# Kernel optimization log

Measured on AMD Instinct MI355X. Metric: run time of the kernel, lower is better.

Reference implementation:

```python
import jax, jax.numpy as jnp
import numpy as np

WINDOW = 33  # must match init_kwargs window_size (odd)


def setup_inputs() -> dict:
    key = jax.random.key(0)
    kq, kk, kv, km = jax.random.split(key, 4)
    B, S, D = 4, 2048, 256
    query = jax.random.normal(kq, (B, S, D), dtype=jnp.float32)
    k = jax.random.normal(kk, (B, S, D), dtype=jnp.float32)
    value = jax.random.normal(kv, (B, S, D), dtype=jnp.float32)
    mask = jax.random.randint(km, (B, S), 0, 2).astype(jnp.int32)
    return {"query": query, "key": k, "value": value, "mask": mask}


def reference(query, key, value, mask):
    # Local (sliding-window) attention, window centered at each position.
    B, S, D = query.shape
    half = WINDOW // 2
    offs = jnp.arange(-half, half + 1)                 # [W]
    idx = jnp.arange(S)[:, None] + offs[None, :]       # [S, W]
    valid = (idx >= 0) & (idx < S)                     # in-bounds window entries
    idxc = jnp.clip(idx, 0, S - 1)
    k_win = key[:, idxc]                               # [B, S, W, D]
    v_win = value[:, idxc]                             # [B, S, W, D]
    scores = jnp.einsum('bsd,bswd->bsw', query, k_win) / jnp.sqrt(jnp.float32(D))
    m_win = (mask[:, idxc] != 0) & valid[None]         # [B, S, W]
    scores = jnp.where(m_win, scores, jnp.float32(-1e10))  # masked_fill(-1e10)
    p_attn = jax.nn.softmax(scores, axis=-1)           # [B, S, W]
    values = jnp.einsum('bsw,bswd->bsd', p_attn, v_win)
    return values, p_attn
```

## Files before the change

kernel.cpp:

```cpp
#include <hip/hip_runtime.h>

#define S_LEN 2048
#define D_DIM 256
#define WIN 33
#define HALF 16
#define TROWS 16
#define SPAN 48
#define SC_STRIDE 68
#define PT_STRIDE 72

typedef __attribute__((ext_vector_type(8))) short short8_t;
typedef __attribute__((ext_vector_type(4))) float f32x4;

__device__ inline unsigned short f32_to_bf16(float f) {
    unsigned u = __float_as_uint(f);
    return (unsigned short)((u + 0x7fffu + ((u >> 16) & 1u)) >> 16);
}
__device__ inline unsigned pack2_bf16(float lo, float hi) {
    unsigned a = __float_as_uint(lo) + 0x8000u;
    unsigned b = __float_as_uint(hi) + 0x8000u;
    return __builtin_amdgcn_perm(b, a, 0x07060302);
}
__device__ inline short8_t pack_bf16x8(float4 x, float4 y) {
    union { unsigned u[4]; short8_t s; } r;
    r.u[0] = pack2_bf16(x.x, x.y); r.u[1] = pack2_bf16(x.z, x.w);
    r.u[2] = pack2_bf16(y.x, y.y); r.u[3] = pack2_bf16(y.z, y.w);
    return r.s;
}

__global__ __launch_bounds__(512) void local_attn_v7(
    const float* __restrict__ q,
    const float* __restrict__ k,
    const float* __restrict__ v,
    const int*   __restrict__ mask,
    float* __restrict__ out_v,
    float* __restrict__ out_p)
{
    __shared__ __align__(16) float          Sc[TROWS * SC_STRIDE];
    __shared__ __align__(16) unsigned short Pt[TROWS * PT_STRIDE];
    __shared__ int wm[SPAN];

    const int t    = threadIdx.x;
    const int lane = t & 63;
    const int w    = t >> 6;
    const int l15  = lane & 15;
    const int q4   = lane >> 4;

    const int bid  = blockIdx.x;
    const int tile = ((bid & 7) << 6) | (bid >> 3);
    const int b    = tile >> 7;
    const int s0   = (tile & 127) << 4;

    const float* qb = q + ((size_t)b * S_LEN + s0) * D_DIM;
    const float* kb = k + (size_t)b * S_LEN * D_DIM;
    const float* vb = v + (size_t)b * S_LEN * D_DIM;

    if (t < SPAN) {
        const int idx = s0 - HALF + t;
        wm[t] = (idx >= 0 && idx < S_LEN) ? (mask[b * S_LEN + idx] != 0) : 0;
    }

    if (w < 3) {
        const int c    = 16 * w + l15;
        const int kidx = min(max(s0 - HALF + c, 0), S_LEN - 1);
        const float* kr = kb + (size_t)kidx * D_DIM;
        const float* qr = qb + (size_t)l15 * D_DIM;
        f32x4 acc = (f32x4){0.f, 0.f, 0.f, 0.f};
#pragma unroll
        for (int ks = 0; ks < 8; ++ks) {
            const float* pq = qr + ks * 32 + q4 * 8;
            const float* pk = kr + ks * 32 + q4 * 8;
            const short8_t aq = pack_bf16x8(*(const float4*)pq, *(const float4*)(pq + 4));
            const short8_t bk = pack_bf16x8(*(const float4*)pk, *(const float4*)(pk + 4));
            acc = __builtin_amdgcn_mfma_f32_16x16x32_bf16(aq, bk, acc, 0, 0, 0);
        }
#pragma unroll
        for (int r = 0; r < 4; ++r)
            Sc[(q4 * 4 + r) * SC_STRIDE + c] = acc[r];
    }

    short8_t bv[2][2];
    {
        const bool act1 = (q4 < 2);
        const short8_t zfrag = {0,0,0,0,0,0,0,0};
        float vr[2][2][8];
#pragma unroll
        for (int nt = 0; nt < 2; ++nt) {
            const int d = 32 * w + nt * 16 + l15;
#pragma unroll
            for (int j = 0; j < 8; ++j) {
                const int g0   = q4 * 8 + j;
                const int idx0 = min(max(s0 - HALF + g0, 0), S_LEN - 1);
                vr[nt][0][j] = vb[(size_t)idx0 * D_DIM + d];
            }
            if (act1) {
#pragma unroll
                for (int j = 0; j < 8; ++j) {
                    const int g1   = 32 + q4 * 8 + j;
                    const int idx1 = min(max(s0 - HALF + g1, 0), S_LEN - 1);
                    vr[nt][1][j] = vb[(size_t)idx1 * D_DIM + d];
                }
            }
        }
#pragma unroll
        for (int nt = 0; nt < 2; ++nt) {
            float4 x, y;
            x.x = vr[nt][0][0]; x.y = vr[nt][0][1]; x.z = vr[nt][0][2]; x.w = vr[nt][0][3];
            y.x = vr[nt][0][4]; y.y = vr[nt][0][5]; y.z = vr[nt][0][6]; y.w = vr[nt][0][7];
            bv[nt][0] = pack_bf16x8(x, y);
            if (act1) {
                x.x = vr[nt][1][0]; x.y = vr[nt][1][1]; x.z = vr[nt][1][2]; x.w = vr[nt][1][3];
                y.x = vr[nt][1][4]; y.y = vr[nt][1][5]; y.z = vr[nt][1][6]; y.w = vr[nt][1][7];
                bv[nt][1] = pack_bf16x8(x, y);
            } else {
                bv[nt][1] = zfrag;
            }
        }
    }
    __syncthreads();

    {
        const int row = t >> 5;
        const int e   = t & 31;
        float vs[2];
#pragma unroll
        for (int kq = 0; kq < 2; ++kq) {
            const int c = 2 * e + kq;
            const int j = c - row;
            const bool inb = (j >= 0) && (j < WIN) && (c < SPAN);
            vs[kq] = inb ? (wm[c < SPAN ? c : 0] ? Sc[row * SC_STRIDE + (c < SPAN ? c : 0)] * 0.0625f
                                                 : -1e10f)
                         : -1e30f;
        }
        float m = fmaxf(vs[0], vs[1]);
        m = fmaxf(m, __shfl_xor(m, 1, 64));
        m = fmaxf(m, __shfl_xor(m, 2, 64));
        m = fmaxf(m, __shfl_xor(m, 4, 64));
        m = fmaxf(m, __shfl_xor(m, 8, 64));
        m = fmaxf(m, __shfl_xor(m, 16, 64));
        float s = 0.f;
#pragma unroll
        for (int kq = 0; kq < 2; ++kq) { vs[kq] = __expf(vs[kq] - m); s += vs[kq]; }
        s += __shfl_xor(s, 1, 64);
        s += __shfl_xor(s, 2, 64);
        s += __shfl_xor(s, 4, 64);
        s += __shfl_xor(s, 8, 64);
        s += __shfl_xor(s, 16, 64);
        const float rinv = 1.0f / s;

        float p0 = vs[0] * rinv, p1 = vs[1] * rinv;
        *(unsigned*)&Pt[row * PT_STRIDE + 2 * e] = pack2_bf16(p0, p1);
        float* prow = out_p + ((size_t)(b * S_LEN + s0 + row)) * WIN;
        const int j0 = 2 * e - row;
        if (j0 >= 0 && j0 < WIN)     prow[j0]     = p0;
        if (j0 + 1 >= 0 && j0 + 1 < WIN) prow[j0 + 1] = p1;
    }
    __syncthreads();

    {
        const short8_t ap0 = *(const short8_t*)&Pt[l15 * PT_STRIDE + q4 * 8];
        const short8_t ap1 = *(const short8_t*)&Pt[l15 * PT_STRIDE + 32 + q4 * 8];
        float* ob = out_v + ((size_t)b * S_LEN + s0) * D_DIM;
#pragma unroll
        for (int nt = 0; nt < 2; ++nt) {
            f32x4 acc = (f32x4){0.f, 0.f, 0.f, 0.f};
            acc = __builtin_amdgcn_mfma_f32_16x16x32_bf16(ap0, bv[nt][0], acc, 0, 0, 0);
            acc = __builtin_amdgcn_mfma_f32_16x16x32_bf16(ap1, bv[nt][1], acc, 0, 0, 0);
            const int d = 32 * w + nt * 16 + l15;
#pragma unroll
            for (int r = 0; r < 4; ++r)
                ob[(size_t)(q4 * 4 + r) * D_DIM + d] = acc[r];
        }
    }
}

extern "C" void kernel_launch(void* const* d_in, const int* in_sizes, int n_in,
                              void* d_out, int out_size, void* d_ws, size_t ws_size,
                              hipStream_t stream) {
    const float* q    = (const float*)d_in[0];
    const float* k    = (const float*)d_in[1];
    const float* v    = (const float*)d_in[2];
    const int*   mask = (const int*)d_in[3];

    const int B = 4;
    float* out_v = (float*)d_out;
    float* out_p = (float*)d_out + (size_t)B * S_LEN * D_DIM;

    const int blocks = B * (S_LEN / TROWS);
    local_attn_v7<<<blocks, 512, 0, stream>>>(q, k, v, mask, out_v, out_p);
}
```

Before: 83.31 us.

## Overlap V loads with softmax via LDS-only barriers and interior fast path

Replaces __syncthreads with a barrier that waits only on LDS traffic, so V global loads issued before the softmax stay in flight across it. The bf16 packing of V moves to after the softmax, where the data is first needed. Interior tiles get a separate path without index clamping, and launch bounds now request 4 blocks per CU. This is meant to hide global-load latency behind the score and softmax work, at the cost of more live registers holding raw V values and a duplicated code path.

```diff
diff --git a/kernel.cpp b/kernel.cpp
--- a/kernel.cpp
+++ b/kernel.cpp
@@ -12,10 +12,6 @@
 typedef __attribute__((ext_vector_type(8))) short short8_t;
 typedef __attribute__((ext_vector_type(4))) float f32x4;
 
-__device__ inline unsigned short f32_to_bf16(float f) {
-    unsigned u = __float_as_uint(f);
-    return (unsigned short)((u + 0x7fffu + ((u >> 16) & 1u)) >> 16);
-}
 __device__ inline unsigned pack2_bf16(float lo, float hi) {
     unsigned a = __float_as_uint(lo) + 0x8000u;
     unsigned b = __float_as_uint(hi) + 0x8000u;
@@ -28,7 +24,11 @@
     return r.s;
 }
 
-__global__ __launch_bounds__(512) void local_attn_v7(
+__device__ inline void lds_barrier() {
+    asm volatile("s_waitcnt lgkmcnt(0)\n\ts_barrier" ::: "memory");
+}
+
+__global__ __launch_bounds__(512, 4) void local_attn_v8(
     const float* __restrict__ q,
     const float* __restrict__ k,
     const float* __restrict__ v,
@@ -49,7 +49,9 @@
     const int bid  = blockIdx.x;
     const int tile = ((bid & 7) << 6) | (bid >> 3);
     const int b    = tile >> 7;
-    const int s0   = (tile & 127) << 4;
+    const int ts   = tile & 127;
+    const int s0   = ts << 4;
+    const bool interior = (ts >= 1) && (ts <= 126);
 
     const float* qb = q + ((size_t)b * S_LEN + s0) * D_DIM;
     const float* kb = k + (size_t)b * S_LEN * D_DIM;
@@ -60,30 +62,60 @@
         wm[t] = (idx >= 0 && idx < S_LEN) ? (mask[b * S_LEN + idx] != 0) : 0;
     }
 
-    if (w < 3) {
-        const int c    = 16 * w + l15;
-        const int kidx = min(max(s0 - HALF + c, 0), S_LEN - 1);
-        const float* kr = kb + (size_t)kidx * D_DIM;
-        const float* qr = qb + (size_t)l15 * D_DIM;
-        f32x4 acc = (f32x4){0.f, 0.f, 0.f, 0.f};
-#pragma unroll
-        for (int ks = 0; ks < 8; ++ks) {
-            const float* pq = qr + ks * 32 + q4 * 8;
-            const float* pk = kr + ks * 32 + q4 * 8;
-            const short8_t aq = pack_bf16x8(*(const float4*)pq, *(const float4*)(pq + 4));
-            const short8_t bk = pack_bf16x8(*(const float4*)pk, *(const float4*)(pk + 4));
-            acc = __builtin_amdgcn_mfma_f32_16x16x32_bf16(aq, bk, acc, 0, 0, 0);
-        }
-#pragma unroll
-        for (int r = 0; r < 4; ++r)
-            Sc[(q4 * 4 + r) * SC_STRIDE + c] = acc[r];
-    }
-
-    short8_t bv[2][2];
-    {
-        const bool act1 = (q4 < 2);
-        const short8_t zfrag = {0,0,0,0,0,0,0,0};
-        float vr[2][2][8];
+    float vr[2][2][8];
+    const bool act1 = (q4 < 2);
+
+    if (interior) {
+        if (w < 3) {
+            const int c = 16 * w + l15;
+            const float* kr = kb + (size_t)(s0 - HALF + c) * D_DIM;
+            const float* qr = qb + (size_t)l15 * D_DIM;
+            f32x4 acc = (f32x4){0.f, 0.f, 0.f, 0.f};
+#pragma unroll
+            for (int ks = 0; ks < 8; ++ks) {
+                const float* pq = qr + ks * 32 + q4 * 8;
+                const float* pk = kr + ks * 32 + q4 * 8;
+                const short8_t aq = pack_bf16x8(*(const float4*)pq, *(const float4*)(pq + 4));
+                const short8_t bk = pack_bf16x8(*(const float4*)pk, *(const float4*)(pk + 4));
+                acc = __builtin_amdgcn_mfma_f32_16x16x32_bf16(aq, bk, acc, 0, 0, 0);
+            }
+#pragma unroll
+            for (int r = 0; r < 4; ++r)
+                Sc[(q4 * 4 + r) * SC_STRIDE + c] = acc[r];
+        }
+        const float* pv = vb + (size_t)(s0 - HALF + q4 * 8) * D_DIM + 32 * w + l15;
+#pragma unroll
+        for (int nt = 0; nt < 2; ++nt) {
+            const float* p0 = pv + nt * 16;
+#pragma unroll
+            for (int j = 0; j < 8; ++j)
+                vr[nt][0][j] = p0[(size_t)j * D_DIM];
+            if (act1) {
+                const float* p1 = p0 + (size_t)32 * D_DIM;
+#pragma unroll
+                for (int j = 0; j < 8; ++j)
+                    vr[nt][1][j] = p1[(size_t)j * D_DIM];
+            }
+        }
+    } else {
+        if (w < 3) {
+            const int c    = 16 * w + l15;
+            const int kidx = min(max(s0 - HALF + c, 0), S_LEN - 1);
+            const float* kr = kb + (size_t)kidx * D_DIM;
+            const float* qr = qb + (size_t)l15 * D_DIM;
+            f32x4 acc = (f32x4){0.f, 0.f, 0.f, 0.f};
+#pragma unroll
+            for (int ks = 0; ks < 8; ++ks) {
+                const float* pq = qr + ks * 32 + q4 * 8;
+                const float* pk = kr + ks * 32 + q4 * 8;
+                const short8_t aq = pack_bf16x8(*(const float4*)pq, *(const float4*)(pq + 4));
+                const short8_t bk = pack_bf16x8(*(const float4*)pk, *(const float4*)(pk + 4));
+                acc = __builtin_amdgcn_mfma_f32_16x16x32_bf16(aq, bk, acc, 0, 0, 0);
+            }
+#pragma unroll
+            for (int r = 0; r < 4; ++r)
+                Sc[(q4 * 4 + r) * SC_STRIDE + c] = acc[r];
+        }
 #pragma unroll
         for (int nt = 0; nt < 2; ++nt) {
             const int d = 32 * w + nt * 16 + l15;
@@ -102,6 +134,52 @@
                 }
             }
         }
+    }
+
+    lds_barrier();
+
+    {
+        const int row = t >> 5;
+        const int e   = t & 31;
+        float vs[2];
+#pragma unroll
+        for (int kq = 0; kq < 2; ++kq) {
+            const int c = 2 * e + kq;
+            const int j = c - row;
+            const bool inb = (j >= 0) && (j < WIN) && (c < SPAN);
+            vs[kq] = inb ? (wm[c < SPAN ? c : 0] ? Sc[row * SC_STRIDE + (c < SPAN ? c : 0)] * 0.0625f
+                                                 : -1e10f)
+                         : -1e30f;
+        }
+        float m = fmaxf(vs[0], vs[1]);
+        m = fmaxf(m, __shfl_xor(m, 1, 64));
+        m = fmaxf(m, __shfl_xor(m, 2, 64));
+        m = fmaxf(m, __shfl_xor(m, 4, 64));
+        m = fmaxf(m, __shfl_xor(m, 8, 64));
+        m = fmaxf(m, __shfl_xor(m, 16, 64));
+        float s = 0.f;
+#pragma unroll
+        for (int kq = 0; kq < 2; ++kq) { vs[kq] = __expf(vs[kq] - m); s += vs[kq]; }
+        s += __shfl_xor(s, 1, 64);
+        s += __shfl_xor(s, 2, 64);
+        s += __shfl_xor(s, 4, 64);
+        s += __shfl_xor(s, 8, 64);
+        s += __shfl_xor(s, 16, 64);
+        const float rinv = 1.0f / s;
+
+        float p0 = vs[0] * rinv, p1 = vs[1] * rinv;
+        *(unsigned*)&Pt[row * PT_STRIDE + 2 * e] = pack2_bf16(p0, p1);
+        float* prow = out_p + ((size_t)(b * S_LEN + s0 + row)) * WIN;
+        const int j0 = 2 * e - row;
+        if (j0 >= 0 && j0 < WIN)         prow[j0]     = p0;
+        if (j0 + 1 >= 0 && j0 + 1 < WIN) prow[j0 + 1] = p1;
+    }
+
+    lds_barrier();
+
+    {
+        const short8_t zfrag = {0, 0, 0, 0, 0, 0, 0, 0};
+        short8_t bv[2][2];
 #pragma unroll
         for (int nt = 0; nt < 2; ++nt) {
             float4 x, y;
@@ -116,48 +194,7 @@
                 bv[nt][1] = zfrag;
             }
         }
-    }
-    __syncthreads();
-
-    {
-        const int row = t >> 5;
-        const int e   = t & 31;
-        float vs[2];
-#pragma unroll
-        for (int kq = 0; kq < 2; ++kq) {
-            const int c = 2 * e + kq;
-            const int j = c - row;
-            const bool inb = (j >= 0) && (j < WIN) && (c < SPAN);
-            vs[kq] = inb ? (wm[c < SPAN ? c : 0] ? Sc[row * SC_STRIDE + (c < SPAN ? c : 0)] * 0.0625f
-                                                 : -1e10f)
-                         : -1e30f;
-        }
-        float m = fmaxf(vs[0], vs[1]);
-        m = fmaxf(m, __shfl_xor(m, 1, 64));
-        m = fmaxf(m, __shfl_xor(m, 2, 64));
-        m = fmaxf(m, __shfl_xor(m, 4, 64));
-        m = fmaxf(m, __shfl_xor(m, 8, 64));
-        m = fmaxf(m, __shfl_xor(m, 16, 64));
-        float s = 0.f;
-#pragma unroll
-        for (int kq = 0; kq < 2; ++kq) { vs[kq] = __expf(vs[kq] - m); s += vs[kq]; }
-        s += __shfl_xor(s, 1, 64);
-        s += __shfl_xor(s, 2, 64);
-        s += __shfl_xor(s, 4, 64);
-        s += __shfl_xor(s, 8, 64);
-        s += __shfl_xor(s, 16, 64);
-        const float rinv = 1.0f / s;
-
-        float p0 = vs[0] * rinv, p1 = vs[1] * rinv;
-        *(unsigned*)&Pt[row * PT_STRIDE + 2 * e] = pack2_bf16(p0, p1);
-        float* prow = out_p + ((size_t)(b * S_LEN + s0 + row)) * WIN;
-        const int j0 = 2 * e - row;
-        if (j0 >= 0 && j0 < WIN)     prow[j0]     = p0;
-        if (j0 + 1 >= 0 && j0 + 1 < WIN) prow[j0 + 1] = p1;
-    }
-    __syncthreads();
-
-    {
+
         const short8_t ap0 = *(const short8_t*)&Pt[l15 * PT_STRIDE + q4 * 8];
         const short8_t ap1 = *(const short8_t*)&Pt[l15 * PT_STRIDE + 32 + q4 * 8];
         float* ob = out_v + ((size_t)b * S_LEN + s0) * D_DIM;
@@ -187,5 +224,5 @@
     float* out_p = (float*)d_out + (size_t)B * S_LEN * D_DIM;
 
     const int blocks = B * (S_LEN / TROWS);
-    local_attn_v7<<<blocks, 512, 0, stream>>>(q, k, v, mask, out_v, out_p);
-}
+    local_attn_v8<<<blocks, 512, 0, stream>>>(q, k, v, mask, out_v, out_p);
+}
```

Result: no change. 84.03 us (+0.9%).
